# Kernel optimization log

Hardware: AMD Instinct MI355X
Metric: run time of the kernel (lower is better)

Reference implementation:

```python
import jax, jax.numpy as jnp
import numpy as np

N = 100000
E = 3200000
IN_DIM = 256
OUT_DIM = 256
BN_EPS = 1e-5


def setup_inputs() -> dict:
    key = jax.random.key(0)
    k1, k2, k3, k4, k5 = jax.random.split(key, 5)
    x = jax.random.normal(k1, (N, IN_DIM), dtype=jnp.float32)
    edge_rows = jax.random.randint(k2, (E,), 0, N, dtype=jnp.int32)
    edge_cols = jax.random.randint(k3, (E,), 0, N, dtype=jnp.int32)
    edge_vals = jax.random.uniform(k4, (E,), dtype=jnp.float32)
    # xavier_uniform-like init for weight
    limit = float(np.sqrt(6.0 / (IN_DIM + OUT_DIM)))
    weight = jax.random.uniform(k5, (IN_DIM, OUT_DIM), minval=-limit, maxval=limit, dtype=jnp.float32)
    gamma = jnp.ones((OUT_DIM,), dtype=jnp.float32)
    beta = jnp.zeros((OUT_DIM,), dtype=jnp.float32)
    return {"x": x, "edge_rows": edge_rows, "edge_cols": edge_cols,
            "edge_vals": edge_vals, "weight": weight, "gamma": gamma, "beta": beta}


def reference(x, edge_rows, edge_cols, edge_vals, weight, gamma, beta):
    # dense projection: [N, in] @ [in, out] -> [N, out]
    z = jnp.matmul(x, weight)
    # sparse adjacency matmul (spmm): gather source rows, scale, scatter-add to dest
    msgs = edge_vals[:, None] * z[edge_cols]          # [E, out]
    agg = jax.ops.segment_sum(msgs, edge_rows, num_segments=N)  # [N, out]
    # BatchNorm1d (training mode: batch stats, biased variance) + ReLU
    mean = jnp.mean(agg, axis=0)
    var = jnp.mean(jnp.square(agg - mean), axis=0)
    norm = (agg - mean) * jax.lax.rsqrt(var + BN_EPS) * gamma + beta
    return jax.nn.relu(norm)
```

## Files before the change

kernel.cpp:

```cpp
#include <hip/hip_runtime.h>
#include <hip/hip_bf16.h>

#define N_NODES 100000
#define N_EDGES 3200000
#define DIM 256
#define BN_EPS 1e-5f
#define BROWS 256
#define NBUCK ((N_NODES + BROWS - 1) / BROWS)
#define BIN_BLOCKS 512
#define EPB (N_EDGES / BIN_BLOCKS)
#define RPW 4
#define NPART 64

typedef __attribute__((ext_vector_type(8))) short short8v;
typedef __attribute__((ext_vector_type(4))) float f32x4;

__device__ __forceinline__ float b2f(unsigned short h) {
    return __uint_as_float(((unsigned int)h) << 16);
}
__device__ __forceinline__ unsigned short f2b(float f) {
    unsigned int u = __float_as_uint(f);
    unsigned int rounded = u + 0x7FFF + ((u >> 16) & 1);
    return (unsigned short)(rounded >> 16);
}

__global__ __launch_bounds__(256) void wfrag_kernel(const float* __restrict__ W,
                                                    unsigned short* __restrict__ wfrag) {
    const int t = blockIdx.x * 256 + threadIdx.x;
    const int e = t & 7;
    const int l = (t >> 3) & 63;
    const int frag = t >> 9;
    const int nt = frag >> 3;
    const int ks = frag & 7;
    const int k = ks * 32 + ((l >> 4) << 3) + e;
    const int c = nt * 16 + (l & 15);
    wfrag[t] = f2b(W[k * DIM + c]);
}

__global__ __launch_bounds__(256) void gemm_mfma_kernel(const float* __restrict__ x,
                                                        const unsigned short* __restrict__ wfrag,
                                                        unsigned short* __restrict__ zb) {
    const int wid = (blockIdx.x * blockDim.x + threadIdx.x) >> 6;
    const int lane = threadIdx.x & 63;
    if (wid >= N_NODES / 16) return;
    const int m0 = wid * 16;

    const int arow = m0 + (lane & 15);
    const int kb = (lane >> 4) << 3;
    const float* xrow = x + (size_t)arow * DIM + kb;
    short8v af[8];
    #pragma unroll
    for (int ks = 0; ks < 8; ++ks) {
        const float4 a0 = *(const float4*)(xrow + ks * 32);
        const float4 a1 = *(const float4*)(xrow + ks * 32 + 4);
        short8v f;
        f[0] = (short)f2b(a0.x); f[1] = (short)f2b(a0.y);
        f[2] = (short)f2b(a0.z); f[3] = (short)f2b(a0.w);
        f[4] = (short)f2b(a1.x); f[5] = (short)f2b(a1.y);
        f[6] = (short)f2b(a1.z); f[7] = (short)f2b(a1.w);
        af[ks] = f;
    }

    const int drow0 = m0 + ((lane >> 4) << 2);
    const int dcol = lane & 15;
    for (int nt = 0; nt < 16; ++nt) {
        f32x4 acc = {0.f, 0.f, 0.f, 0.f};
        const unsigned short* wp = wfrag + ((size_t)(nt * 8) * 64 + lane) * 8;
        #pragma unroll
        for (int ks = 0; ks < 8; ++ks) {
            const short8v bf = *(const short8v*)(wp + (size_t)ks * 64 * 8);
            acc = __builtin_amdgcn_mfma_f32_16x16x32_bf16(af[ks], bf, acc, 0, 0, 0);
        }
        unsigned short* zp = zb + (size_t)drow0 * DIM + nt * 16 + dcol;
        zp[0]       = f2b(acc[0]);
        zp[DIM]     = f2b(acc[1]);
        zp[2 * DIM] = f2b(acc[2]);
        zp[3 * DIM] = f2b(acc[3]);
    }
}

__global__ __launch_bounds__(256) void coarse_hist_kernel(const int* __restrict__ rows,
                                                          int* __restrict__ coarse) {
    __shared__ int h[NBUCK];
    const int t = threadIdx.x;
    for (int i = t; i < NBUCK; i += 256) h[i] = 0;
    __syncthreads();
    const int stride = gridDim.x * 256;
    for (int e = blockIdx.x * 256 + t; e < N_EDGES; e += stride)
        atomicAdd(&h[rows[e] >> 8], 1);
    __syncthreads();
    for (int i = t; i < NBUCK; i += 256)
        if (h[i]) atomicAdd(&coarse[i], h[i]);
}

__global__ __launch_bounds__(512) void scan_coarse_kernel(const int* __restrict__ coarse,
                                                          int* __restrict__ coarseBase,
                                                          int* __restrict__ gCursor,
                                                          int* __restrict__ row_ptr) {
    __shared__ int s[512];
    const int t = threadIdx.x;
    const int v = (t < NBUCK) ? coarse[t] : 0;
    s[t] = v;
    __syncthreads();
    for (int off = 1; off < 512; off <<= 1) {
        int x = (t >= off) ? s[t - off] : 0;
        __syncthreads();
        s[t] += x;
        __syncthreads();
    }
    if (t < NBUCK) {
        coarseBase[t] = s[t] - v;
        gCursor[t] = s[t] - v;
    }
    if (t == 0) row_ptr[N_NODES] = N_EDGES;
}

__global__ __launch_bounds__(256) void bin_kernel(const int* __restrict__ rows,
                                                  const int* __restrict__ cols,
                                                  const float* __restrict__ vals,
                                                  int* gCursor,
                                                  int2* __restrict__ gBinned) {
    __shared__ int h[NBUCK];
    __shared__ int base[NBUCK];
    __shared__ int cur[NBUCK];
    const int t = threadIdx.x;
    const int e0 = blockIdx.x * EPB;
    for (int i = t; i < NBUCK; i += 256) h[i] = 0;
    __syncthreads();
    for (int e = e0 + t; e < e0 + EPB; e += 256)
        atomicAdd(&h[rows[e] >> 8], 1);
    __syncthreads();
    for (int b = t; b < NBUCK; b += 256) {
        cur[b] = 0;
        if (h[b]) base[b] = atomicAdd(&gCursor[b], h[b]);
    }
    __syncthreads();
    for (int e = e0 + t; e < e0 + EPB; e += 256) {
        const int r = rows[e];
        const int b = r >> 8;
        const int rk = atomicAdd(&cur[b], 1);
        int2 p;
        p.x = ((r & 255) << 17) | cols[e];
        p.y = __float_as_int(vals[e]);
        gBinned[base[b] + rk] = p;
    }
}

__global__ __launch_bounds__(256) void fine_sort_kernel(const int* __restrict__ coarse,
                                                        const int* __restrict__ coarseBase,
                                                        const int2* __restrict__ gBinned,
                                                        int* __restrict__ row_ptr,
                                                        int2* __restrict__ finalE) {
    __shared__ int h[BROWS];
    __shared__ int s[BROWS];
    __shared__ int cur[BROWS];
    const int t = threadIdx.x;
    const int b = blockIdx.x;
    const int base0 = coarseBase[b];
    const int cnt = coarse[b];
    h[t] = 0;
    __syncthreads();
    for (int e = base0 + t; e < base0 + cnt; e += 256)
        atomicAdd(&h[gBinned[e].x >> 17], 1);
    __syncthreads();
    s[t] = h[t];
    __syncthreads();
    for (int off = 1; off < BROWS; off <<= 1) {
        int x = (t >= off) ? s[t - off] : 0;
        __syncthreads();
        s[t] += x;
        __syncthreads();
    }
    const int excl = s[t] - h[t];
    const int grow = b * BROWS + t;
    if (grow < N_NODES) row_ptr[grow] = base0 + excl;
    cur[t] = excl;
    __syncthreads();
    for (int e = base0 + t; e < base0 + cnt; e += 256) {
        const int2 p = gBinned[e];
        const int rl = p.x >> 17;
        const int rk = atomicAdd(&cur[rl], 1);
        int2 q;
        q.x = p.x & 0x1FFFF;
        q.y = p.y;
        finalE[base0 + rk] = q;
    }
}

__global__ __launch_bounds__(256) void spmm_csr_kernel(const int* __restrict__ row_ptr,
                                                       const int2* __restrict__ pairs,
                                                       const unsigned short* __restrict__ zb,
                                                       float* __restrict__ out,
                                                       float* __restrict__ partials) {
    __shared__ float sdata[2 * DIM];
    const int t = threadIdx.x;
    sdata[t] = 0.f;
    sdata[t + 256] = 0.f;
    __syncthreads();

    const int wave = (blockIdx.x * 256 + t) >> 6;
    const int lane = t & 63;
    const int row0 = wave * RPW;

    float4 s  = make_float4(0.f, 0.f, 0.f, 0.f);
    float4 sq = make_float4(0.f, 0.f, 0.f, 0.f);

    for (int row = row0; row < row0 + RPW; ++row) {
        const int start = __builtin_amdgcn_readfirstlane(row_ptr[row]);
        const int end   = __builtin_amdgcn_readfirstlane(row_ptr[row + 1]);
        float4 acc = make_float4(0.f, 0.f, 0.f, 0.f);
        int e = start;
        for (; e + 8 <= end; e += 8) {
            int2 p[8];
            #pragma unroll
            for (int j = 0; j < 8; ++j) p[j] = pairs[e + j];
            ushort4 m[8];
            #pragma unroll
            for (int j = 0; j < 8; ++j)
                m[j] = ((const ushort4*)(zb + (size_t)p[j].x * DIM))[lane];
            #pragma unroll
            for (int j = 0; j < 8; ++j) {
                const float v = __int_as_float(p[j].y);
                acc.x += v * b2f(m[j].x);
                acc.y += v * b2f(m[j].y);
                acc.z += v * b2f(m[j].z);
                acc.w += v * b2f(m[j].w);
            }
        }
        for (; e < end; ++e) {
            const int2 p0 = pairs[e];
            const float v0 = __int_as_float(p0.y);
            const ushort4 m0 = ((const ushort4*)(zb + (size_t)p0.x * DIM))[lane];
            acc.x += v0 * b2f(m0.x);
            acc.y += v0 * b2f(m0.y);
            acc.z += v0 * b2f(m0.z);
            acc.w += v0 * b2f(m0.w);
        }
        ((float4*)(out + (size_t)row * DIM))[lane] = acc;
        s.x += acc.x; s.y += acc.y; s.z += acc.z; s.w += acc.w;
        sq.x += acc.x * acc.x; sq.y += acc.y * acc.y;
        sq.z += acc.z * acc.z; sq.w += acc.w * acc.w;
    }

    const int c0 = lane * 4;
    atomicAdd(&sdata[c0 + 0], s.x);
    atomicAdd(&sdata[c0 + 1], s.y);
    atomicAdd(&sdata[c0 + 2], s.z);
    atomicAdd(&sdata[c0 + 3], s.w);
    atomicAdd(&sdata[256 + c0 + 0], sq.x);
    atomicAdd(&sdata[256 + c0 + 1], sq.y);
    atomicAdd(&sdata[256 + c0 + 2], sq.z);
    atomicAdd(&sdata[256 + c0 + 3], sq.w);
    __syncthreads();

    float* pb = partials + (size_t)(blockIdx.x & (NPART - 1)) * (2 * DIM);
    atomicAdd(&pb[t], sdata[t]);
    atomicAdd(&pb[t + 256], sdata[t + 256]);
}

__global__ __launch_bounds__(256) void finalize_kernel(const float* __restrict__ partials,
                                                       const float* __restrict__ gamma,
                                                       const float* __restrict__ beta,
                                                       float* __restrict__ sb) {
    const int c = threadIdx.x;
    float s = 0.f, ssq = 0.f;
    for (int b = 0; b < NPART; ++b) {
        s   += partials[b * (2 * DIM) + c];
        ssq += partials[b * (2 * DIM) + 256 + c];
    }
    const float inv_n = 1.0f / (float)N_NODES;
    const float mean = s * inv_n;
    float var = ssq * inv_n - mean * mean;
    const float rstd = rsqrtf(var + BN_EPS);
    const float scale = rstd * gamma[c];
    sb[c] = scale;
    sb[DIM + c] = beta[c] - mean * scale;
}

#define NORM_BLOCKS 2048
__global__ __launch_bounds__(256) void norm_kernel(float* __restrict__ out,
                                                   const float* __restrict__ sb) {
    const int c0 = (threadIdx.x & 63) * 4;
    const float s0 = sb[c0 + 0], s1 = sb[c0 + 1], s2 = sb[c0 + 2], s3 = sb[c0 + 3];
    const float b0 = sb[DIM + c0 + 0], b1 = sb[DIM + c0 + 1];
    const float b2 = sb[DIM + c0 + 2], b3 = sb[DIM + c0 + 3];
    const int nvec = N_NODES * (DIM / 4);
    for (int idx = blockIdx.x * 256 + threadIdx.x; idx < nvec; idx += NORM_BLOCKS * 256) {
        float4 a = ((float4*)out)[idx];
        float4 o;
        o.x = fmaxf(fmaf(a.x, s0, b0), 0.f);
        o.y = fmaxf(fmaf(a.y, s1, b1), 0.f);
        o.z = fmaxf(fmaf(a.z, s2, b2), 0.f);
        o.w = fmaxf(fmaf(a.w, s3, b3), 0.f);
        ((float4*)out)[idx] = o;
    }
}

extern "C" void kernel_launch(void* const* d_in, const int* in_sizes, int n_in,
                              void* d_out, int out_size, void* d_ws, size_t ws_size,
                              hipStream_t stream) {
    const float* x         = (const float*)d_in[0];
    const int*   edge_rows = (const int*)d_in[1];
    const int*   edge_cols = (const int*)d_in[2];
    const float* edge_vals = (const float*)d_in[3];
    const float* weight    = (const float*)d_in[4];
    const float* gamma     = (const float*)d_in[5];
    const float* beta      = (const float*)d_in[6];
    float* out = (float*)d_out;

    unsigned short* zb    = (unsigned short*)d_ws;
    unsigned short* wfrag = zb + (size_t)N_NODES * DIM;
    int2*  gBinned  = (int2*)(wfrag + DIM * DIM);
    int2*  finalE   = gBinned + N_EDGES;
    int*   row_ptr  = (int*)(finalE + N_EDGES);
    int*   coarse   = row_ptr + N_NODES + 1;
    float* partials = (float*)(coarse + 392);
    float* sb       = partials + NPART * 2 * DIM;
    int*   coarseBase = (int*)(sb + 2 * DIM);
    int*   gCursor  = coarseBase + 392;

    hipMemsetAsync(coarse, 0, (392 + NPART * 2 * DIM) * sizeof(int), stream);

    wfrag_kernel<<<DIM * DIM / 256, 256, 0, stream>>>(weight, wfrag);
    gemm_mfma_kernel<<<(N_NODES / 16 + 3) / 4, 256, 0, stream>>>(x, wfrag, zb);

    coarse_hist_kernel<<<BIN_BLOCKS, 256, 0, stream>>>(edge_rows, coarse);
    scan_coarse_kernel<<<1, 512, 0, stream>>>(coarse, coarseBase, gCursor, row_ptr);
    bin_kernel<<<BIN_BLOCKS, 256, 0, stream>>>(edge_rows, edge_cols, edge_vals, gCursor, gBinned);
    fine_sort_kernel<<<NBUCK, 256, 0, stream>>>(coarse, coarseBase, gBinned, row_ptr, finalE);

    spmm_csr_kernel<<<N_NODES / (RPW * 4), 256, 0, stream>>>(row_ptr, finalE, zb, out, partials);

    finalize_kernel<<<1, 256, 0, stream>>>(partials, gamma, beta, sb);
    norm_kernel<<<NORM_BLOCKS, 256, 0, stream>>>(out, sb);
}
```

Baseline: 487.0 us.

## Assign one row per wave and double-buffer edge gathers in SpMM

The SpMM kernel now gives each wave a single row instead of four and launches four times as many blocks. The edge loop is software-pipelined with two register buffers, so the next batch of eight gathers is issued while the current batch is being accumulated. The scalar tail loop becomes one predicated batch. This aims for more memory-level parallelism and better latency hiding on the random row gathers, at the cost of more registers, more blocks, and four times as many shared and global atomics for the BatchNorm statistics.

```diff
diff --git a/kernel.cpp b/kernel.cpp
--- a/kernel.cpp
+++ b/kernel.cpp
@@ -9,7 +9,6 @@
 #define NBUCK ((N_NODES + BROWS - 1) / BROWS)
 #define BIN_BLOCKS 512
 #define EPB (N_EDGES / BIN_BLOCKS)
-#define RPW 4
 #define NPART 64
 
 typedef __attribute__((ext_vector_type(8))) short short8v;
@@ -198,59 +197,79 @@
     sdata[t + 256] = 0.f;
     __syncthreads();
 
-    const int wave = (blockIdx.x * 256 + t) >> 6;
+    const int row  = (blockIdx.x * 256 + t) >> 6;
     const int lane = t & 63;
-    const int row0 = wave * RPW;
-
-    float4 s  = make_float4(0.f, 0.f, 0.f, 0.f);
-    float4 sq = make_float4(0.f, 0.f, 0.f, 0.f);
-
-    for (int row = row0; row < row0 + RPW; ++row) {
-        const int start = __builtin_amdgcn_readfirstlane(row_ptr[row]);
-        const int end   = __builtin_amdgcn_readfirstlane(row_ptr[row + 1]);
-        float4 acc = make_float4(0.f, 0.f, 0.f, 0.f);
-        int e = start;
-        for (; e + 8 <= end; e += 8) {
-            int2 p[8];
-            #pragma unroll
-            for (int j = 0; j < 8; ++j) p[j] = pairs[e + j];
-            ushort4 m[8];
-            #pragma unroll
-            for (int j = 0; j < 8; ++j)
-                m[j] = ((const ushort4*)(zb + (size_t)p[j].x * DIM))[lane];
-            #pragma unroll
-            for (int j = 0; j < 8; ++j) {
-                const float v = __int_as_float(p[j].y);
-                acc.x += v * b2f(m[j].x);
-                acc.y += v * b2f(m[j].y);
-                acc.z += v * b2f(m[j].z);
-                acc.w += v * b2f(m[j].w);
-            }
+    const int start = __builtin_amdgcn_readfirstlane(row_ptr[row]);
+    const int end   = __builtin_amdgcn_readfirstlane(row_ptr[row + 1]);
+
+    float4 acc = make_float4(0.f, 0.f, 0.f, 0.f);
+    int2 pA[8], pB[8];
+    ushort4 mA[8], mB[8];
+
+#define LOADX(P, M, EB) do { \
+    _Pragma("unroll") for (int j = 0; j < 8; ++j) P[j] = pairs[(EB) + j]; \
+    _Pragma("unroll") for (int j = 0; j < 8; ++j) \
+        M[j] = ((const ushort4*)(zb + (size_t)P[j].x * DIM))[lane]; \
+  } while (0)
+#define FMAX(P, M) do { \
+    _Pragma("unroll") for (int j = 0; j < 8; ++j) { \
+        const float v = __int_as_float(P[j].y); \
+        acc.x += v * b2f(M[j].x); \
+        acc.y += v * b2f(M[j].y); \
+        acc.z += v * b2f(M[j].z); \
+        acc.w += v * b2f(M[j].w); \
+    } \
+  } while (0)
+
+    const int nb = (end - start) >> 3;
+    int e = start;
+    if (nb) {
+        LOADX(pA, mA, e); e += 8;
+        int b = 1;
+        for (; b + 1 < nb; b += 2) {
+            LOADX(pB, mB, e); e += 8;
+            FMAX(pA, mA);
+            LOADX(pA, mA, e); e += 8;
+            FMAX(pB, mB);
         }
-        for (; e < end; ++e) {
-            const int2 p0 = pairs[e];
-            const float v0 = __int_as_float(p0.y);
-            const ushort4 m0 = ((const ushort4*)(zb + (size_t)p0.x * DIM))[lane];
-            acc.x += v0 * b2f(m0.x);
-            acc.y += v0 * b2f(m0.y);
-            acc.z += v0 * b2f(m0.z);
-            acc.w += v0 * b2f(m0.w);
+        if (b < nb) {
+            LOADX(pB, mB, e); e += 8;
+            FMAX(pA, mA);
+            FMAX(pB, mB);
+        } else {
+            FMAX(pA, mA);
         }
-        ((float4*)(out + (size_t)row * DIM))[lane] = acc;
-        s.x += acc.x; s.y += acc.y; s.z += acc.z; s.w += acc.w;
-        sq.x += acc.x * acc.x; sq.y += acc.y * acc.y;
-        sq.z += acc.z * acc.z; sq.w += acc.w * acc.w;
-    }
+    }
+    const int rem = end - e;
+    if (rem) {
+        #pragma unroll
+        for (int j = 0; j < 8; ++j) if (j < rem) pA[j] = pairs[e + j];
+        #pragma unroll
+        for (int j = 0; j < 8; ++j) if (j < rem)
+            mA[j] = ((const ushort4*)(zb + (size_t)pA[j].x * DIM))[lane];
+        #pragma unroll
+        for (int j = 0; j < 8; ++j) if (j < rem) {
+            const float v = __int_as_float(pA[j].y);
+            acc.x += v * b2f(mA[j].x);
+            acc.y += v * b2f(mA[j].y);
+            acc.z += v * b2f(mA[j].z);
+            acc.w += v * b2f(mA[j].w);
+        }
+    }
+#undef LOADX
+#undef FMAX
+
+    ((float4*)(out + (size_t)row * DIM))[lane] = acc;
 
     const int c0 = lane * 4;
-    atomicAdd(&sdata[c0 + 0], s.x);
-    atomicAdd(&sdata[c0 + 1], s.y);
-    atomicAdd(&sdata[c0 + 2], s.z);
-    atomicAdd(&sdata[c0 + 3], s.w);
-    atomicAdd(&sdata[256 + c0 + 0], sq.x);
-    atomicAdd(&sdata[256 + c0 + 1], sq.y);
-    atomicAdd(&sdata[256 + c0 + 2], sq.z);
-    atomicAdd(&sdata[256 + c0 + 3], sq.w);
+    atomicAdd(&sdata[c0 + 0], acc.x);
+    atomicAdd(&sdata[c0 + 1], acc.y);
+    atomicAdd(&sdata[c0 + 2], acc.z);
+    atomicAdd(&sdata[c0 + 3], acc.w);
+    atomicAdd(&sdata[256 + c0 + 0], acc.x * acc.x);
+    atomicAdd(&sdata[256 + c0 + 1], acc.y * acc.y);
+    atomicAdd(&sdata[256 + c0 + 2], acc.z * acc.z);
+    atomicAdd(&sdata[256 + c0 + 3], acc.w * acc.w);
     __syncthreads();
 
     float* pb = partials + (size_t)(blockIdx.x & (NPART - 1)) * (2 * DIM);
@@ -329,7 +348,7 @@
     bin_kernel<<<BIN_BLOCKS, 256, 0, stream>>>(edge_rows, edge_cols, edge_vals, gCursor, gBinned);
     fine_sort_kernel<<<NBUCK, 256, 0, stream>>>(coarse, coarseBase, gBinned, row_ptr, finalE);
 
-    spmm_csr_kernel<<<N_NODES / (RPW * 4), 256, 0, stream>>>(row_ptr, finalE, zb, out, partials);
+    spmm_csr_kernel<<<N_NODES / 4, 256, 0, stream>>>(row_ptr, finalE, zb, out, partials);
 
     finalize_kernel<<<1, 256, 0, stream>>>(partials, gamma, beta, sb);
     norm_kernel<<<NORM_BLOCKS, 256, 0, stream>>>(out, sb);
```

After: 563.9 us. 1.16x slower.

## Use one wave per row in 1024-thread SpMM blocks with nontemporal edge loads

Applied to the files above, without the earlier changes.

Restructures the CSR SpMM so each wave handles one row instead of four, with 16 rows per 1024-thread block. The edge unroll drops from 8 to 4, and edge pairs and output rows now use nontemporal loads and stores. The goal is more parallelism and more memory requests in flight for the random gathers, without polluting the cache with streamed data. The trade-off is more LDS atomics per block for the batch-norm statistics, and fewer independent gathers in flight per wave.

```diff
diff --git a/kernel.cpp b/kernel.cpp
--- a/kernel.cpp
+++ b/kernel.cpp
@@ -9,11 +9,11 @@
 #define NBUCK ((N_NODES + BROWS - 1) / BROWS)
 #define BIN_BLOCKS 512
 #define EPB (N_EDGES / BIN_BLOCKS)
-#define RPW 4
 #define NPART 64
 
 typedef __attribute__((ext_vector_type(8))) short short8v;
 typedef __attribute__((ext_vector_type(4))) float f32x4;
+typedef __attribute__((ext_vector_type(2))) int i32x2;
 
 __device__ __forceinline__ float b2f(unsigned short h) {
     return __uint_as_float(((unsigned int)h) << 16);
@@ -187,75 +187,68 @@
     }
 }
 
-__global__ __launch_bounds__(256) void spmm_csr_kernel(const int* __restrict__ row_ptr,
-                                                       const int2* __restrict__ pairs,
-                                                       const unsigned short* __restrict__ zb,
-                                                       float* __restrict__ out,
-                                                       float* __restrict__ partials) {
+__global__ __launch_bounds__(1024) void spmm_csr_kernel(const int* __restrict__ row_ptr,
+                                                        const int2* __restrict__ pairs,
+                                                        const unsigned short* __restrict__ zb,
+                                                        float* __restrict__ out,
+                                                        float* __restrict__ partials) {
     __shared__ float sdata[2 * DIM];
     const int t = threadIdx.x;
-    sdata[t] = 0.f;
-    sdata[t + 256] = 0.f;
-    __syncthreads();
-
-    const int wave = (blockIdx.x * 256 + t) >> 6;
+    if (t < 2 * DIM) sdata[t] = 0.f;
+    __syncthreads();
+
+    const int row  = blockIdx.x * 16 + (t >> 6);
     const int lane = t & 63;
-    const int row0 = wave * RPW;
-
-    float4 s  = make_float4(0.f, 0.f, 0.f, 0.f);
-    float4 sq = make_float4(0.f, 0.f, 0.f, 0.f);
-
-    for (int row = row0; row < row0 + RPW; ++row) {
-        const int start = __builtin_amdgcn_readfirstlane(row_ptr[row]);
-        const int end   = __builtin_amdgcn_readfirstlane(row_ptr[row + 1]);
-        float4 acc = make_float4(0.f, 0.f, 0.f, 0.f);
-        int e = start;
-        for (; e + 8 <= end; e += 8) {
-            int2 p[8];
-            #pragma unroll
-            for (int j = 0; j < 8; ++j) p[j] = pairs[e + j];
-            ushort4 m[8];
-            #pragma unroll
-            for (int j = 0; j < 8; ++j)
-                m[j] = ((const ushort4*)(zb + (size_t)p[j].x * DIM))[lane];
-            #pragma unroll
-            for (int j = 0; j < 8; ++j) {
-                const float v = __int_as_float(p[j].y);
-                acc.x += v * b2f(m[j].x);
-                acc.y += v * b2f(m[j].y);
-                acc.z += v * b2f(m[j].z);
-                acc.w += v * b2f(m[j].w);
-            }
-        }
-        for (; e < end; ++e) {
-            const int2 p0 = pairs[e];
-            const float v0 = __int_as_float(p0.y);
-            const ushort4 m0 = ((const ushort4*)(zb + (size_t)p0.x * DIM))[lane];
-            acc.x += v0 * b2f(m0.x);
-            acc.y += v0 * b2f(m0.y);
-            acc.z += v0 * b2f(m0.z);
-            acc.w += v0 * b2f(m0.w);
-        }
-        ((float4*)(out + (size_t)row * DIM))[lane] = acc;
-        s.x += acc.x; s.y += acc.y; s.z += acc.z; s.w += acc.w;
-        sq.x += acc.x * acc.x; sq.y += acc.y * acc.y;
-        sq.z += acc.z * acc.z; sq.w += acc.w * acc.w;
-    }
+    const int start = row_ptr[row];
+    const int end   = row_ptr[row + 1];
+
+    const i32x2* pp = (const i32x2*)pairs;
+    float4 acc = make_float4(0.f, 0.f, 0.f, 0.f);
+    int e = start;
+    for (; e + 3 < end; e += 4) {
+        const i32x2 p0 = __builtin_nontemporal_load(pp + e);
+        const i32x2 p1 = __builtin_nontemporal_load(pp + e + 1);
+        const i32x2 p2 = __builtin_nontemporal_load(pp + e + 2);
+        const i32x2 p3 = __builtin_nontemporal_load(pp + e + 3);
+        const float v0 = __int_as_float(p0.y), v1 = __int_as_float(p1.y);
+        const float v2 = __int_as_float(p2.y), v3 = __int_as_float(p3.y);
+        const ushort4 m0 = ((const ushort4*)(zb + (size_t)p0.x * DIM))[lane];
+        const ushort4 m1 = ((const ushort4*)(zb + (size_t)p1.x * DIM))[lane];
+        const ushort4 m2 = ((const ushort4*)(zb + (size_t)p2.x * DIM))[lane];
+        const ushort4 m3 = ((const ushort4*)(zb + (size_t)p3.x * DIM))[lane];
+        acc.x += v0 * b2f(m0.x) + v1 * b2f(m1.x) + v2 * b2f(m2.x) + v3 * b2f(m3.x);
+        acc.y += v0 * b2f(m0.y) + v1 * b2f(m1.y) + v2 * b2f(m2.y) + v3 * b2f(m3.y);
+        acc.z += v0 * b2f(m0.z) + v1 * b2f(m1.z) + v2 * b2f(m2.z) + v3 * b2f(m3.z);
+        acc.w += v0 * b2f(m0.w) + v1 * b2f(m1.w) + v2 * b2f(m2.w) + v3 * b2f(m3.w);
+    }
+    for (; e < end; ++e) {
+        const i32x2 p0 = __builtin_nontemporal_load(pp + e);
+        const float v0 = __int_as_float(p0.y);
+        const ushort4 m0 = ((const ushort4*)(zb + (size_t)p0.x * DIM))[lane];
+        acc.x += v0 * b2f(m0.x);
+        acc.y += v0 * b2f(m0.y);
+        acc.z += v0 * b2f(m0.z);
+        acc.w += v0 * b2f(m0.w);
+    }
+
+    f32x4 st = {acc.x, acc.y, acc.z, acc.w};
+    __builtin_nontemporal_store(st, (f32x4*)(out + (size_t)row * DIM) + lane);
 
     const int c0 = lane * 4;
-    atomicAdd(&sdata[c0 + 0], s.x);
-    atomicAdd(&sdata[c0 + 1], s.y);
-    atomicAdd(&sdata[c0 + 2], s.z);
-    atomicAdd(&sdata[c0 + 3], s.w);
-    atomicAdd(&sdata[256 + c0 + 0], sq.x);
-    atomicAdd(&sdata[256 + c0 + 1], sq.y);
-    atomicAdd(&sdata[256 + c0 + 2], sq.z);
-    atomicAdd(&sdata[256 + c0 + 3], sq.w);
-    __syncthreads();
-
-    float* pb = partials + (size_t)(blockIdx.x & (NPART - 1)) * (2 * DIM);
-    atomicAdd(&pb[t], sdata[t]);
-    atomicAdd(&pb[t + 256], sdata[t + 256]);
+    atomicAdd(&sdata[c0 + 0], acc.x);
+    atomicAdd(&sdata[c0 + 1], acc.y);
+    atomicAdd(&sdata[c0 + 2], acc.z);
+    atomicAdd(&sdata[c0 + 3], acc.w);
+    atomicAdd(&sdata[256 + c0 + 0], acc.x * acc.x);
+    atomicAdd(&sdata[256 + c0 + 1], acc.y * acc.y);
+    atomicAdd(&sdata[256 + c0 + 2], acc.z * acc.z);
+    atomicAdd(&sdata[256 + c0 + 3], acc.w * acc.w);
+    __syncthreads();
+
+    if (t < 2 * DIM) {
+        float* pb = partials + (size_t)(blockIdx.x & (NPART - 1)) * (2 * DIM);
+        atomicAdd(&pb[t], sdata[t]);
+    }
 }
 
 __global__ __launch_bounds__(256) void finalize_kernel(const float* __restrict__ partials,
@@ -329,7 +322,7 @@
     bin_kernel<<<BIN_BLOCKS, 256, 0, stream>>>(edge_rows, edge_cols, edge_vals, gCursor, gBinned);
     fine_sort_kernel<<<NBUCK, 256, 0, stream>>>(coarse, coarseBase, gBinned, row_ptr, finalE);
 
-    spmm_csr_kernel<<<N_NODES / (RPW * 4), 256, 0, stream>>>(row_ptr, finalE, zb, out, partials);
+    spmm_csr_kernel<<<N_NODES / 16, 1024, 0, stream>>>(row_ptr, finalE, zb, out, partials);
 
     finalize_kernel<<<1, 256, 0, stream>>>(partials, gamma, beta, sb);
     norm_kernel<<<NORM_BLOCKS, 256, 0, stream>>>(out, sb);
```

Result: slower. 640.5 us (+31.5%).
